# Optimization experiments

Measured on AMD Instinct MI355X. Metric: run time of the kernel, lower is better.

Reference implementation:

```python
import jax, jax.numpy as jnp
import numpy as np

NODE_DIM = 64  # Net.node_dim


def _peg_conv(x, pos, edge_index, W, b, em_w, em_b):
    """PEGConv: GCN norm (with self-loops) + positional edge gate sigmoid(Linear(1,1)(sqdist))."""
    n = x.shape[0]
    loop = jnp.arange(n)
    row = jnp.concatenate([edge_index[0], loop])  # source j (with self-loops)
    col = jnp.concatenate([edge_index[1], loop])  # target i
    ones = jnp.ones(row.shape[0], dtype=x.dtype)
    deg = jax.ops.segment_sum(ones, col, num_segments=n)
    dinv = jnp.where(deg > 0, jax.lax.rsqrt(deg), 0.0)
    norm = dinv[row] * dinv[col]                                       # [E+N]
    h = x @ W                                                          # [N, out]
    sq = jnp.sum((pos[col] - pos[row]) ** 2, axis=-1, keepdims=True)   # [E+N, 1]
    gate = jax.nn.sigmoid(sq * em_w[0, 0] + em_b[0])                   # edge MLP Linear(1,1)+Sigmoid
    msg = gate * (norm[:, None] * h[row])                              # [E+N, out]
    return jax.ops.segment_sum(msg, col, num_segments=n) + b


def setup_inputs() -> dict:
    key = jax.random.key(0)
    ks = jax.random.split(key, 12)
    N, E_MP, E_LP = 50000, 800000, 100000
    IN, POS, HID = 128, 32, 64
    return {
        "x": jax.random.normal(ks[0], (N, IN), jnp.float32),
        "pos": jax.random.normal(ks[1], (N, POS), jnp.float32),
        "pos_edge_index": jax.random.randint(ks[2], (2, E_LP), 0, N),
        "neg_edge_index": jax.random.randint(ks[3], (2, E_LP), 0, N),
        "train_pos": jax.random.randint(ks[4], (2, E_MP), 0, N),
        "W1": jax.random.normal(ks[5], (IN, HID), jnp.float32) / np.float32(np.sqrt(IN)),
        "b1": jnp.zeros((HID,), jnp.float32),
        "em1_w": jax.random.normal(ks[6], (1, 1), jnp.float32),
        "em1_b": jnp.zeros((1,), jnp.float32),
        "W2": jax.random.normal(ks[7], (HID, HID), jnp.float32) / np.float32(np.sqrt(HID)),
        "b2": jnp.zeros((HID,), jnp.float32),
        "em2_w": jax.random.normal(ks[8], (1, 1), jnp.float32),
        "em2_b": jnp.zeros((1,), jnp.float32),
        "fc_w": jax.random.normal(ks[9], (1, 2), jnp.float32),  # nn.Linear(2,1) weight
        "fc_b": jnp.zeros((1,), jnp.float32),
    }


def reference(x, pos, pos_edge_index, neg_edge_index, train_pos,
              W1, b1, em1_w, em1_b, W2, b2, em2_w, em2_b, fc_w, fc_b):
    edge_index = jnp.concatenate([pos_edge_index, neg_edge_index], axis=-1)  # [2, 2*E_LP]
    h = _peg_conv(x, pos, train_pos, W1, b1, em1_w, em1_b)
    h = _peg_conv(h, pos, train_pos, W2, b2, em2_w, em2_b)
    nodes_first = h[edge_index[0], :NODE_DIM]
    nodes_second = h[edge_index[1], :NODE_DIM]
    pe = jnp.sum((pos[edge_index[0]] - pos[edge_index[1]]) ** 2, axis=-1, keepdims=True)
    pred = jnp.sum(nodes_first * nodes_second, axis=-1, keepdims=True)
    feats = jnp.concatenate([pred, pe], axis=1)  # [2*E_LP, 2]
    return feats @ fc_w.T + fc_b                 # [2*E_LP, 1]
```

## Files before the change

### kernel.cpp

```cpp
#include <hip/hip_runtime.h>

#define HID 64
#define POS_DIM 32
#define IN_DIM 128

__device__ __forceinline__ float fsig(float v) {
    return 1.0f / (1.0f + __expf(-v));
}

__device__ __forceinline__ unsigned short f2bf(float f) {
    unsigned int u = __float_as_uint(f);
    u = u + 0x7FFFu + ((u >> 16) & 1u);
    return (unsigned short)(u >> 16);
}
__device__ __forceinline__ float bf2f(unsigned short s) {
    return __uint_as_float(((unsigned int)s) << 16);
}
__device__ __forceinline__ float2 bfpair(unsigned int u) {
    return make_float2(__uint_as_float(u << 16),
                       __uint_as_float(u & 0xFFFF0000u));
}

__global__ __launch_bounds__(256) void k_pre(const int* __restrict__ tp,
                                             const float* __restrict__ pos,
                                             int* cnt, float* __restrict__ sq,
                                             int* __restrict__ rank, int E) {
    int lane = threadIdx.x & 63;
    int wid  = threadIdx.x >> 6;
    int sub  = lane >> 3;
    int j    = lane & 7;
    int e = (blockIdx.x * 4 + wid) * 8 + sub;
    if (e >= E) return;
    int row = tp[e];
    int col = tp[E + e];
    float4 a = ((const float4*)(pos + (size_t)row * POS_DIM))[j];
    float4 b = ((const float4*)(pos + (size_t)col * POS_DIM))[j];
    float dx = a.x - b.x, dy = a.y - b.y, dz = a.z - b.z, dw = a.w - b.w;
    float s = 0.0f;
    s = fmaf(dx, dx, s); s = fmaf(dy, dy, s);
    s = fmaf(dz, dz, s); s = fmaf(dw, dw, s);
    s += __shfl_xor(s, 1);
    s += __shfl_xor(s, 2);
    s += __shfl_xor(s, 4);
    if (j == 0) {
        sq[e] = s;
        rank[e] = atomicAdd(&cnt[col], 1);
    }
}

__global__ __launch_bounds__(256) void k_bsum(const int* __restrict__ cnt,
                                              int* __restrict__ bsum, int n) {
    int i = blockIdx.x * 256 + threadIdx.x;
    int v = (i < n) ? cnt[i] : 0;
    #pragma unroll
    for (int o = 32; o; o >>= 1) v += __shfl_down(v, o);
    __shared__ int w[4];
    int lane = threadIdx.x & 63, wid = threadIdx.x >> 6;
    if (lane == 0) w[wid] = v;
    __syncthreads();
    if (threadIdx.x == 0) bsum[blockIdx.x] = w[0] + w[1] + w[2] + w[3];
}

__global__ __launch_bounds__(256) void k_scan2(const int* __restrict__ cnt,
                                               const int* __restrict__ bsum,
                                               int* __restrict__ off,
                                               float* __restrict__ dinv,
                                               int n, int Etot) {
    __shared__ int s[256];
    __shared__ int wsum[4];
    int tid = threadIdx.x, bid = blockIdx.x;
    int p = 0;
    for (int t = tid; t < bid; t += 256) p += bsum[t];
    #pragma unroll
    for (int o = 32; o; o >>= 1) p += __shfl_down(p, o);
    int lane = tid & 63, wid = tid >> 6;
    if (lane == 0) wsum[wid] = p;
    __syncthreads();
    int bpre = wsum[0] + wsum[1] + wsum[2] + wsum[3];
    int i = bid * 256 + tid;
    int v = (i < n) ? cnt[i] : 0;
    s[tid] = v;
    __syncthreads();
    #pragma unroll
    for (int d = 1; d < 256; d <<= 1) {
        int t_ = (tid >= d) ? s[tid - d] : 0;
        __syncthreads();
        s[tid] += t_;
        __syncthreads();
    }
    if (i < n) {
        off[i]  = bpre + s[tid] - v;
        dinv[i] = rsqrtf((float)(v + 1));
    }
    if (i == 0) off[n] = Etot;
}

__global__ __launch_bounds__(256) void k_fill(const int* __restrict__ tp,
                                              const int* __restrict__ off,
                                              const int* __restrict__ rank,
                                              const float* __restrict__ sq,
                                              const float* __restrict__ dinv,
                                              const float* em1w, const float* em1b,
                                              const float* em2w, const float* em2b,
                                              int4* __restrict__ csr, int E) {
    int e = blockIdx.x * blockDim.x + threadIdx.x;
    if (e >= E) return;
    int row = tp[e];
    int col = tp[E + e];
    int slot = off[col] + rank[e];
    float nrm = dinv[row] * dinv[col];
    float s = sq[e];
    float c1 = fsig(s * em1w[0] + em1b[0]) * nrm;
    float c2 = fsig(s * em2w[0] + em2b[0]) * nrm;
    csr[slot] = make_int4(row, __float_as_int(c1), __float_as_int(c2), 0);
}

template<int K>
__global__ __launch_bounds__(256) void k_gemm(const float* __restrict__ X,
                                              const float* __restrict__ W,
                                              unsigned short* __restrict__ H, int n) {
    constexpr int KP = K + 4;
    __shared__ float Ws[K * HID];
    __shared__ float Xs[32 * KP];
    int tid = threadIdx.x;
    const float4* W4 = (const float4*)W;
    float4* Ws4 = (float4*)Ws;
    for (int i = tid; i < K * HID / 4; i += 256) Ws4[i] = W4[i];
    int row0 = blockIdx.x * 32;
    for (int i = tid; i < 32 * K / 4; i += 256) {
        int r  = i / (K / 4);
        int kv = i % (K / 4);
        float4 v = make_float4(0.f, 0.f, 0.f, 0.f);
        if (row0 + r < n) v = ((const float4*)(X + (size_t)(row0 + r) * K))[kv];
        ((float4*)(Xs + r * KP))[kv] = v;
    }
    __syncthreads();
    int cg = tid & 15;  int col0 = cg * 4;
    int rg = tid >> 4;  int r0 = rg * 2;
    float acc[2][4] = {};
    for (int k = 0; k < K; ++k) {
        float4 w = *(const float4*)(Ws + k * HID + col0);
        float x0 = Xs[r0 * KP + k];
        float x1 = Xs[(r0 + 1) * KP + k];
        acc[0][0] = fmaf(x0, w.x, acc[0][0]); acc[0][1] = fmaf(x0, w.y, acc[0][1]);
        acc[0][2] = fmaf(x0, w.z, acc[0][2]); acc[0][3] = fmaf(x0, w.w, acc[0][3]);
        acc[1][0] = fmaf(x1, w.x, acc[1][0]); acc[1][1] = fmaf(x1, w.y, acc[1][1]);
        acc[1][2] = fmaf(x1, w.z, acc[1][2]); acc[1][3] = fmaf(x1, w.w, acc[1][3]);
    }
    #pragma unroll
    for (int rr = 0; rr < 2; ++rr) {
        int row = row0 + r0 + rr;
        if (row < n) {
            ushort4 o;
            o.x = f2bf(acc[rr][0]); o.y = f2bf(acc[rr][1]);
            o.z = f2bf(acc[rr][2]); o.w = f2bf(acc[rr][3]);
            *(ushort4*)(H + (size_t)row * HID + col0) = o;
        }
    }
}

template<bool BF16OUT>
__global__ __launch_bounds__(256) void k_agg(const int* __restrict__ off,
                                             const int4* __restrict__ csr,
                                             const unsigned short* __restrict__ h,
                                             const float* __restrict__ dinv,
                                             const float* __restrict__ bias,
                                             const float* emb,
                                             void* __restrict__ outv, int n,
                                             int layer) {
    int wid  = threadIdx.x >> 6;
    int lane = threadIdx.x & 63;
    int i = blockIdx.x * 4 + wid;
    if (i >= n) return;
    float di = dinv[i];
    float gself = fsig(emb[0]);
    float acc = bias[lane] + gself * di * di * bf2f(h[(size_t)i * HID + lane]);
    int s = off[i], s1 = off[i + 1];
    for (; s + 4 <= s1; s += 4) {
        int4 e0 = csr[s],     e1 = csr[s + 1];
        int4 e2 = csr[s + 2], e3 = csr[s + 3];
        float c0 = __int_as_float(layer ? e0.z : e0.y);
        float c1 = __int_as_float(layer ? e1.z : e1.y);
        float c2 = __int_as_float(layer ? e2.z : e2.y);
        float c3 = __int_as_float(layer ? e3.z : e3.y);
        float v0 = bf2f(h[(size_t)e0.x * HID + lane]);
        float v1 = bf2f(h[(size_t)e1.x * HID + lane]);
        float v2 = bf2f(h[(size_t)e2.x * HID + lane]);
        float v3 = bf2f(h[(size_t)e3.x * HID + lane]);
        acc = fmaf(c0, v0, acc); acc = fmaf(c1, v1, acc);
        acc = fmaf(c2, v2, acc); acc = fmaf(c3, v3, acc);
    }
    for (; s < s1; ++s) {
        int4 e0 = csr[s];
        acc = fmaf(__int_as_float(layer ? e0.z : e0.y),
                   bf2f(h[(size_t)e0.x * HID + lane]), acc);
    }
    if (BF16OUT) ((unsigned short*)outv)[(size_t)i * HID + lane] = f2bf(acc);
    else         ((float*)outv)[(size_t)i * HID + lane] = acc;
}

__global__ __launch_bounds__(256) void k_predict(const int* __restrict__ pei,
                                                 const int* __restrict__ nei,
                                                 const unsigned short* __restrict__ h,
                                                 const float* __restrict__ pos,
                                                 const float* fcw, const float* fcb,
                                                 float* __restrict__ out, int Elp) {
    int j = threadIdx.x & 7;
    int e = blockIdx.x * 32 + (threadIdx.x >> 3);
    if (e >= 2 * Elp) return;
    int src, dst;
    if (e < Elp) { src = pei[e];        dst = pei[Elp + e]; }
    else         { src = nei[e - Elp];  dst = nei[e];       }
    uint4 hs = ((const uint4*)(h + (size_t)src * HID))[j];
    uint4 hd = ((const uint4*)(h + (size_t)dst * HID))[j];
    float p = 0.0f;
    {
        float2 a, b;
        a = bfpair(hs.x); b = bfpair(hd.x);
        p = fmaf(a.x, b.x, p); p = fmaf(a.y, b.y, p);
        a = bfpair(hs.y); b = bfpair(hd.y);
        p = fmaf(a.x, b.x, p); p = fmaf(a.y, b.y, p);
        a = bfpair(hs.z); b = bfpair(hd.z);
        p = fmaf(a.x, b.x, p); p = fmaf(a.y, b.y, p);
        a = bfpair(hs.w); b = bfpair(hd.w);
        p = fmaf(a.x, b.x, p); p = fmaf(a.y, b.y, p);
    }
    float4 pa = ((const float4*)(pos + (size_t)src * POS_DIM))[j];
    float4 pb = ((const float4*)(pos + (size_t)dst * POS_DIM))[j];
    float dx = pa.x - pb.x, dy = pa.y - pb.y, dz = pa.z - pb.z, dw = pa.w - pb.w;
    float pe = 0.0f;
    pe = fmaf(dx, dx, pe); pe = fmaf(dy, dy, pe);
    pe = fmaf(dz, dz, pe); pe = fmaf(dw, dw, pe);
    p  += __shfl_xor(p, 1);  pe += __shfl_xor(pe, 1);
    p  += __shfl_xor(p, 2);  pe += __shfl_xor(pe, 2);
    p  += __shfl_xor(p, 4);  pe += __shfl_xor(pe, 4);
    if (j == 0) out[e] = fcw[0] * p + fcw[1] * pe + fcb[0];
}

static inline size_t align16(size_t v) { return (v + 15) & ~(size_t)15; }

extern "C" void kernel_launch(void* const* d_in, const int* in_sizes, int n_in,
                              void* d_out, int out_size, void* d_ws, size_t ws_size,
                              hipStream_t stream) {
    const float* x    = (const float*)d_in[0];
    const float* pos  = (const float*)d_in[1];
    const int*   pei  = (const int*)d_in[2];
    const int*   nei  = (const int*)d_in[3];
    const int*   tp   = (const int*)d_in[4];
    const float* W1   = (const float*)d_in[5];
    const float* b1   = (const float*)d_in[6];
    const float* em1w = (const float*)d_in[7];
    const float* em1b = (const float*)d_in[8];
    const float* W2   = (const float*)d_in[9];
    const float* b2   = (const float*)d_in[10];
    const float* em2w = (const float*)d_in[11];
    const float* em2b = (const float*)d_in[12];
    const float* fcw  = (const float*)d_in[13];
    const float* fcb  = (const float*)d_in[14];
    float* outp = (float*)d_out;

    const int N   = in_sizes[0] / IN_DIM;
    const int E   = in_sizes[4] / 2;
    const int Elp = in_sizes[2] / 2;
    const int NB  = (N + 255) / 256;

    char* base = (char*)d_ws;
    size_t o = 0;
    int4* csr = (int4*)(base + o);          o += align16((size_t)E * 16);
    int*   cnt  = (int*)(base + o);         o += align16((size_t)N * 4);
    int*   off  = (int*)(base + o);         o += align16((size_t)(N + 1) * 4);
    int*   bsum = (int*)(base + o);         o += align16((size_t)NB * 4);
    float* dinv = (float*)(base + o);       o += align16((size_t)N * 4);
    float* obuf = (float*)(base + o);       o += align16((size_t)N * HID * 4);
    char*  region = base + o;
    int*   rank = (int*)region;
    float* sq   = (float*)(region + align16((size_t)E * 4));
    unsigned short* hbuf = (unsigned short*)region;

    hipMemsetAsync(cnt, 0, (size_t)N * 4, stream);
    k_pre<<<(E + 31) / 32, 256, 0, stream>>>(tp, pos, cnt, sq, rank, E);
    k_bsum<<<NB, 256, 0, stream>>>(cnt, bsum, N);
    k_scan2<<<NB, 256, 0, stream>>>(cnt, bsum, off, dinv, N, E);
    k_fill<<<(E + 255) / 256, 256, 0, stream>>>(tp, off, rank, sq, dinv,
                                                em1w, em1b, em2w, em2b, csr, E);

    k_gemm<IN_DIM><<<(N + 31) / 32, 256, 0, stream>>>(x, W1, hbuf, N);
    k_agg<false><<<(N + 3) / 4, 256, 0, stream>>>(off, csr, hbuf, dinv, b1, em1b, obuf, N, 0);

    k_gemm<HID><<<(N + 31) / 32, 256, 0, stream>>>(obuf, W2, hbuf, N);
    k_agg<true><<<(N + 3) / 4, 256, 0, stream>>>(off, csr, hbuf, dinv, b2, em2b,
                                                 (void*)obuf, N, 1);

    k_predict<<<(2 * Elp + 31) / 32, 256, 0, stream>>>(pei, nei, (const unsigned short*)obuf,
                                                       pos, fcw, fcb, outp, Elp);
}
```

Before: 218.0 us.

## Use bf16 MFMA for node GEMMs and store layer-1 output in bf16

Replaces the scalar FMA shared-memory GEMM with a 64-row tile kernel that stages X and a transposed W in swizzled LDS as bf16 and runs mfma_f32_16x16x32_bf16. The first aggregation now writes bf16 output, so the second GEMM reads half the bytes. This targets GEMM compute and memory-traffic cost. It rounds the inputs to bf16 before multiplying, which lowers precision, and the output stores are 2-byte scalar writes.

```diff
diff --git a/kernel.cpp b/kernel.cpp
--- a/kernel.cpp
+++ b/kernel.cpp
@@ -3,6 +3,9 @@
 #define HID 64
 #define POS_DIM 32
 #define IN_DIM 128
+
+using short8 = __attribute__((ext_vector_type(8))) short;
+using f32x4  = __attribute__((ext_vector_type(4))) float;
 
 __device__ __forceinline__ float fsig(float v) {
     return 1.0f / (1.0f + __expf(-v));
@@ -19,6 +22,9 @@
 __device__ __forceinline__ float2 bfpair(unsigned int u) {
     return make_float2(__uint_as_float(u << 16),
                        __uint_as_float(u & 0xFFFF0000u));
+}
+__device__ __forceinline__ unsigned int pack2bf(float a, float b) {
+    return (unsigned int)f2bf(a) | ((unsigned int)f2bf(b) << 16);
 }
 
 __global__ __launch_bounds__(256) void k_pre(const int* __restrict__ tp,
@@ -115,46 +121,78 @@
     csr[slot] = make_int4(row, __float_as_int(c1), __float_as_int(c2), 0);
 }
 
-template<int K>
-__global__ __launch_bounds__(256) void k_gemm(const float* __restrict__ X,
-                                              const float* __restrict__ W,
-                                              unsigned short* __restrict__ H, int n) {
-    constexpr int KP = K + 4;
-    __shared__ float Ws[K * HID];
-    __shared__ float Xs[32 * KP];
-    int tid = threadIdx.x;
-    const float4* W4 = (const float4*)W;
-    float4* Ws4 = (float4*)Ws;
-    for (int i = tid; i < K * HID / 4; i += 256) Ws4[i] = W4[i];
-    int row0 = blockIdx.x * 32;
-    for (int i = tid; i < 32 * K / 4; i += 256) {
-        int r  = i / (K / 4);
-        int kv = i % (K / 4);
-        float4 v = make_float4(0.f, 0.f, 0.f, 0.f);
-        if (row0 + r < n) v = ((const float4*)(X + (size_t)(row0 + r) * K))[kv];
-        ((float4*)(Xs + r * KP))[kv] = v;
+template<int K, bool IN_BF16>
+__global__ __launch_bounds__(256) void k_gemm_mfma(const void* __restrict__ Xv,
+                                                   const float* __restrict__ W,
+                                                   unsigned short* __restrict__ H,
+                                                   int n) {
+    constexpr int RB   = K * 2;
+    constexpr int CPR  = K / 8;
+    __shared__ unsigned char lds[64 * RB * 2];
+    unsigned char* As = lds;
+    unsigned char* Bt = lds + 64 * RB;
+
+    int tid  = threadIdx.x;
+    int row0 = blockIdx.x * 64;
+
+    for (int i = tid; i < 64 * CPR; i += 256) {
+        int r  = i / CPR;
+        int kb = i % CPR;
+        uint4 val;
+        if (row0 + r < n) {
+            if (IN_BF16) {
+                val = *(const uint4*)((const unsigned short*)Xv + (size_t)(row0 + r) * K + kb * 8);
+            } else {
+                const float* src = (const float*)Xv + (size_t)(row0 + r) * K + kb * 8;
+                float4 f0 = ((const float4*)src)[0];
+                float4 f1 = ((const float4*)src)[1];
+                val.x = pack2bf(f0.x, f0.y); val.y = pack2bf(f0.z, f0.w);
+                val.z = pack2bf(f1.x, f1.y); val.w = pack2bf(f1.z, f1.w);
+            }
+        } else {
+            val = make_uint4(0, 0, 0, 0);
+        }
+        *(uint4*)(As + r * RB + ((kb ^ (r & 7)) << 4)) = val;
+    }
+    for (int i = tid; i < K * 16; i += 256) {
+        int k  = i / 16;
+        int c0 = (i % 16) * 4;
+        float4 w = ((const float4*)W)[i];
+        #pragma unroll
+        for (int u = 0; u < 4; ++u) {
+            int c = c0 + u;
+            float vv = (u == 0) ? w.x : (u == 1) ? w.y : (u == 2) ? w.z : w.w;
+            int byte = c * RB + ((((k * 2) >> 4) ^ (c & 7)) << 4) + ((k & 7) * 2);
+            *(unsigned short*)(Bt + byte) = f2bf(vv);
+        }
     }
     __syncthreads();
-    int cg = tid & 15;  int col0 = cg * 4;
-    int rg = tid >> 4;  int r0 = rg * 2;
-    float acc[2][4] = {};
-    for (int k = 0; k < K; ++k) {
-        float4 w = *(const float4*)(Ws + k * HID + col0);
-        float x0 = Xs[r0 * KP + k];
-        float x1 = Xs[(r0 + 1) * KP + k];
-        acc[0][0] = fmaf(x0, w.x, acc[0][0]); acc[0][1] = fmaf(x0, w.y, acc[0][1]);
-        acc[0][2] = fmaf(x0, w.z, acc[0][2]); acc[0][3] = fmaf(x0, w.w, acc[0][3]);
-        acc[1][0] = fmaf(x1, w.x, acc[1][0]); acc[1][1] = fmaf(x1, w.y, acc[1][1]);
-        acc[1][2] = fmaf(x1, w.z, acc[1][2]); acc[1][3] = fmaf(x1, w.w, acc[1][3]);
-    }
-    #pragma unroll
-    for (int rr = 0; rr < 2; ++rr) {
-        int row = row0 + r0 + rr;
-        if (row < n) {
-            ushort4 o;
-            o.x = f2bf(acc[rr][0]); o.y = f2bf(acc[rr][1]);
-            o.z = f2bf(acc[rr][2]); o.w = f2bf(acc[rr][3]);
-            *(ushort4*)(H + (size_t)row * HID + col0) = o;
+
+    int wv   = tid >> 6;
+    int lane = tid & 63;
+    int l15  = lane & 15;
+    int g    = lane >> 4;
+
+    f32x4 acc[4] = {{0,0,0,0},{0,0,0,0},{0,0,0,0},{0,0,0,0}};
+    #pragma unroll
+    for (int kk = 0; kk < K / 32; ++kk) {
+        int kc = kk * 4 + g;
+        int arow = wv * 16 + l15;
+        short8 a = *(const short8*)(As + arow * RB + ((kc ^ (arow & 7)) << 4));
+        #pragma unroll
+        for (int cb = 0; cb < 4; ++cb) {
+            int c = cb * 16 + l15;
+            short8 b = *(const short8*)(Bt + c * RB + ((kc ^ (c & 7)) << 4));
+            acc[cb] = __builtin_amdgcn_mfma_f32_16x16x32_bf16(a, b, acc[cb], 0, 0, 0);
+        }
+    }
+
+    #pragma unroll
+    for (int cb = 0; cb < 4; ++cb) {
+        #pragma unroll
+        for (int r = 0; r < 4; ++r) {
+            int row = row0 + wv * 16 + g * 4 + r;
+            if (row < n) H[(size_t)row * HID + cb * 16 + l15] = f2bf(acc[cb][r]);
         }
     }
 }
@@ -271,7 +309,7 @@
     int*   off  = (int*)(base + o);         o += align16((size_t)(N + 1) * 4);
     int*   bsum = (int*)(base + o);         o += align16((size_t)NB * 4);
     float* dinv = (float*)(base + o);       o += align16((size_t)N * 4);
-    float* obuf = (float*)(base + o);       o += align16((size_t)N * HID * 4);
+    unsigned short* obuf = (unsigned short*)(base + o); o += align16((size_t)N * HID * 4);
     char*  region = base + o;
     int*   rank = (int*)region;
     float* sq   = (float*)(region + align16((size_t)E * 4));
@@ -284,13 +322,14 @@
     k_fill<<<(E + 255) / 256, 256, 0, stream>>>(tp, off, rank, sq, dinv,
                                                 em1w, em1b, em2w, em2b, csr, E);
 
-    k_gemm<IN_DIM><<<(N + 31) / 32, 256, 0, stream>>>(x, W1, hbuf, N);
-    k_agg<false><<<(N + 3) / 4, 256, 0, stream>>>(off, csr, hbuf, dinv, b1, em1b, obuf, N, 0);
-
-    k_gemm<HID><<<(N + 31) / 32, 256, 0, stream>>>(obuf, W2, hbuf, N);
+    k_gemm_mfma<IN_DIM, false><<<(N + 63) / 64, 256, 0, stream>>>(x, W1, hbuf, N);
+    k_agg<true><<<(N + 3) / 4, 256, 0, stream>>>(off, csr, hbuf, dinv, b1, em1b,
+                                                 (void*)obuf, N, 0);
+
+    k_gemm_mfma<HID, true><<<(N + 63) / 64, 256, 0, stream>>>(obuf, W2, hbuf, N);
     k_agg<true><<<(N + 3) / 4, 256, 0, stream>>>(off, csr, hbuf, dinv, b2, em2b,
                                                  (void*)obuf, N, 1);
 
-    k_predict<<<(2 * Elp + 31) / 32, 256, 0, stream>>>(pei, nei, (const unsigned short*)obuf,
+    k_predict<<<(2 * Elp + 31) / 32, 256, 0, stream>>>(pei, nei, obuf,
                                                        pos, fcw, fcb, outp, Elp);
 }
```

New measurement: 189.9 us. 12.9% less time.
